# Kernel optimization log

Hardware: AMD Instinct MI355X
Metric: run time of the kernel (lower is better)

The kernel has to match this reference:

```python
import jax, jax.numpy as jnp
import numpy as np

B, N, D = 2, 4096, 512
H, DH = 8, 64  # heads, dim_head; inner_dim = H*DH = 512
SCALE = DH ** -0.5


def setup_inputs() -> dict:
    key = jax.random.key(0)
    ks = jax.random.split(key, 5)
    s = 0.02
    return {
        "x": jax.random.normal(ks[0], (B, N, D), dtype=jnp.float32),
        "Wq": jax.random.normal(ks[1], (D, H * DH), dtype=jnp.float32) * s,
        "Wk": jax.random.normal(ks[2], (D, H * DH), dtype=jnp.float32) * s,
        "Wv": jax.random.normal(ks[3], (D, H * DH), dtype=jnp.float32) * s,
        "Wo": jax.random.normal(ks[4], (H * DH, D), dtype=jnp.float32) * s,
        "bo": jnp.zeros((D,), dtype=jnp.float32),
    }


def reference(x, Wq, Wk, Wv, Wo, bo):
    b, n, _ = x.shape
    # projections (bias-free), then split heads: b n (h d) -> b h n d
    q = (x @ Wq).reshape(b, n, H, DH).transpose(0, 2, 1, 3)
    k = (x @ Wk).reshape(b, n, H, DH).transpose(0, 2, 1, 3)
    v = (x @ Wv).reshape(b, n, H, DH).transpose(0, 2, 1, 3)
    # fp32 QK^T (module upcasts under ATTN_PRECISION='fp32')
    sim = jnp.einsum("bhid,bhjd->bhij", q.astype(jnp.float32), k.astype(jnp.float32)) * SCALE
    attn = jax.nn.softmax(sim, axis=-1)
    out = jnp.einsum("bhij,bhjd->bhid", attn, v)
    # merge heads: b h n d -> b n (h d)
    out = out.transpose(0, 2, 1, 3).reshape(b, n, H * DH)
    return out @ Wo + bo  # dropout p=0 -> identity
```

## Files before the change

kernel.cpp:

```cpp
#include <hip/hip_runtime.h>


typedef __bf16 bf16;
typedef __bf16 bf16x2 __attribute__((ext_vector_type(2)));
typedef __bf16 bf16x4 __attribute__((ext_vector_type(4)));
typedef __bf16 bf16x8 __attribute__((ext_vector_type(8)));
typedef float  f32x2  __attribute__((ext_vector_type(2)));
typedef float  f32x4  __attribute__((ext_vector_type(4)));
typedef float  f32x16 __attribute__((ext_vector_type(16)));

#define MFMA16 __builtin_amdgcn_mfma_f32_16x16x32_bf16
#define MFMA32 __builtin_amdgcn_mfma_f32_32x32x16_bf16

__device__ __forceinline__ int swz(int b) { return b ^ ((b >> 3) & 0x70); }

__device__ __forceinline__ void gload16(const void* g, void* l) {
  __builtin_amdgcn_global_load_lds(
      (const __attribute__((address_space(1))) unsigned int*)g,
      (__attribute__((address_space(3))) unsigned int*)l, 16, 0, 0);
}

__device__ __forceinline__ unsigned pk2(float a, float b) {
  union { bf16x2 h; unsigned u; } x;
  x.h[0] = (bf16)a; x.h[1] = (bf16)b;
  return x.u;
}

__global__ __launch_bounds__(256) void k_cvt(const float* __restrict__ x,
                                             const float* __restrict__ Wq,
                                             const float* __restrict__ Wk,
                                             const float* __restrict__ Wv,
                                             const float* __restrict__ Wo,
                                             bf16* __restrict__ xb,
                                             bf16* __restrict__ Wts) {
  int bid = blockIdx.x;
  if (bid < 4096) {
    int i = (bid * 256 + threadIdx.x) * 4;
    f32x4 v = *(const f32x4*)(x + i);
    bf16x4 o;
    o[0] = (bf16)v[0]; o[1] = (bf16)v[1]; o[2] = (bf16)v[2]; o[3] = (bf16)v[3];
    *(bf16x4*)(xb + i) = o;
  } else {
    int t = (bid - 4096) * 256 + threadIdx.x;
    int w = t >> 18, idx = t & 262143;
    int k = idx >> 9, n = idx & 511;
    const float* W = (w == 0) ? Wq : (w == 1) ? Wk : (w == 2) ? Wv : Wo;
    Wts[(size_t)w * 262144 + n * 512 + k] = (bf16)W[k * 512 + n];
  }
}

__device__ __forceinline__ void gemm_mainloop(const char* Ag, const char* Bg,
                                              char* sA, char* sB, f32x4 acc[4][4]) {
  const int tid = threadIdx.x;
  const int g = (tid >> 4) & 3, lr = tid & 15;
  const int wr = ((tid >> 7) & 1) * 64, wc = ((tid >> 6) & 1) * 64;
  f32x4 zero = {0.f, 0.f, 0.f, 0.f};
#pragma unroll
  for (int mt = 0; mt < 4; mt++)
#pragma unroll
    for (int nt = 0; nt < 4; nt++) acc[mt][nt] = zero;

  for (int k0 = 0; k0 < 512; k0 += 64) {
#pragma unroll
    for (int i = 0; i < 4; i++) {
      int c = i * 256 + tid;
      int row = c >> 3, cl = (c & 7) ^ (row & 7);
      gload16(Ag + row * 1024 + k0 * 2 + cl * 16, sA + (c & ~63) * 16);
    }
#pragma unroll
    for (int i = 0; i < 4; i++) {
      int c = i * 256 + tid;
      int row = c >> 3, cl = (c & 7) ^ (row & 7);
      gload16(Bg + row * 1024 + k0 * 2 + cl * 16, sB + (c & ~63) * 16);
    }
    __syncthreads();
#pragma unroll
    for (int kk = 0; kk < 2; kk++) {
      bf16x8 af[4], bfr[4];
#pragma unroll
      for (int mt = 0; mt < 4; mt++)
        af[mt] = *(const bf16x8*)(sA + swz((wr + mt * 16 + lr) * 128 + kk * 64 + g * 16));
#pragma unroll
      for (int nt = 0; nt < 4; nt++)
        bfr[nt] = *(const bf16x8*)(sB + swz((wc + nt * 16 + lr) * 128 + kk * 64 + g * 16));
#pragma unroll
      for (int mt = 0; mt < 4; mt++)
#pragma unroll
        for (int nt = 0; nt < 4; nt++)
          acc[mt][nt] = MFMA16(af[mt], bfr[nt], acc[mt][nt], 0, 0, 0);
    }
    __syncthreads();
  }
}

__global__ __launch_bounds__(256) void k_gemm_qkv(const bf16* __restrict__ Xb,
                                                  const bf16* __restrict__ Wts,
                                                  bf16* __restrict__ Qo,
                                                  bf16* __restrict__ Ko,
                                                  bf16* __restrict__ Vto) {
  __shared__ __align__(16) char smem[32768];
  const int tid = threadIdx.x;
  const int g = (tid >> 4) & 3, lr = tid & 15;
  const int mb = blockIdx.x * 128, nb = blockIdx.y * 128;
  const int mode = blockIdx.z;
  f32x4 acc[4][4];
  gemm_mainloop((const char*)Xb + (size_t)mb * 1024,
                (const char*)(Wts + (size_t)mode * 262144) + (size_t)nb * 1024,
                smem, smem + 16384, acc);
  const int wr = ((tid >> 7) & 1) * 64, wc = ((tid >> 6) & 1) * 64;
  const float qs = 0.18033688011112042f;
#pragma unroll
  for (int mt = 0; mt < 4; mt++)
#pragma unroll
    for (int nt = 0; nt < 4; nt++)
#pragma unroll
      for (int r = 0; r < 4; r++) {
        int m = mb + wr + mt * 16 + g * 4 + r;
        int cc = nb + wc + nt * 16 + lr;
        float v = acc[mt][nt][r];
        int b = m >> 12, ns = m & 4095, h = cc >> 6, d = cc & 63;
        if (mode == 0)
          Qo[((size_t)(b * 8 + h) * 4096 + ns) * 64 + d] = (bf16)(v * qs);
        else if (mode == 1)
          Ko[((size_t)(b * 8 + h) * 4096 + ns) * 64 + d] = (bf16)v;
        else
          Vto[((size_t)(b * 8 + h) * 64 + d) * 4096 + ns] = (bf16)v;
      }
}

__global__ __launch_bounds__(256) void k_gemm_out(const bf16* __restrict__ Ob,
                                                  const bf16* __restrict__ WtO,
                                                  const float* __restrict__ bo,
                                                  float* __restrict__ out) {
  __shared__ __align__(16) char smem[32768];
  const int tid = threadIdx.x;
  const int g = (tid >> 4) & 3, lr = tid & 15;
  const int mb = blockIdx.x * 128, nb = blockIdx.y * 128;
  f32x4 acc[4][4];
  gemm_mainloop((const char*)Ob + (size_t)mb * 1024,
                (const char*)WtO + (size_t)nb * 1024, smem, smem + 16384, acc);
  const int wr = ((tid >> 7) & 1) * 64, wc = ((tid >> 6) & 1) * 64;
#pragma unroll
  for (int mt = 0; mt < 4; mt++)
#pragma unroll
    for (int nt = 0; nt < 4; nt++)
#pragma unroll
      for (int r = 0; r < 4; r++) {
        int m = mb + wr + mt * 16 + g * 4 + r;
        int cc = nb + wc + nt * 16 + lr;
        out[(size_t)m * 512 + cc] = acc[mt][nt][r] + bo[cc];
      }
}

__global__ __launch_bounds__(512, 4) void k_attn(const bf16* __restrict__ Q,
                                                 const bf16* __restrict__ K,
                                                 const bf16* __restrict__ Vt,
                                                 bf16* __restrict__ O) {
  __shared__ __align__(16) char smem[65536];
  const int tid = threadIdx.x;
  const int l = tid & 63, w = tid >> 6, lo = l & 31, hi = l >> 5;
  const int strip = w & 3, half = w >> 2;
  const int tid2 = tid & 255;
  const int bh = blockIdx.y;
  const int q0 = blockIdx.x * 128 + strip * 32;
  const char* Qp = (const char*)Q + ((size_t)bh * 4096 + q0 + lo) * 128;
  bf16x8 qf[4];
#pragma unroll
  for (int ks = 0; ks < 4; ks++) qf[ks] = *(const bf16x8*)(Qp + ks * 32 + hi * 16);

  const int srow = tid2 >> 3, scl = (tid2 & 7) ^ (srow & 7);
  const char* pK0 = (const char*)K + (size_t)bh * 4096 * 128 +
                    (size_t)half * 2048 * 128 + srow * 128 + scl * 16;
  const char* pV0 = (const char*)Vt + (size_t)bh * 64 * 8192 +
                    (size_t)half * 4096 + (size_t)srow * 8192 + scl * 16;
  char* lbase = smem + half * 32768;
  const int sdst = (tid2 & ~63) * 16;

  const int offR = swz(lo * 128 + hi * 16);

  f32x16 acc0 = {}, acc1 = {};
  const f32x16 z16 = {};
  float lsum = 0.f;

  {
    char* d = lbase + sdst;
    gload16(pK0, d);
    gload16(pK0 + 4096, d + 4096);
    gload16(pV0, d + 8192);
    gload16(pV0 + 262144, d + 12288);
  }
  pK0 += 8192; pV0 += 128;
  __syncthreads();

  for (int t = 0; t < 32; t++) {
    if (t < 31) {
      char* d = lbase + ((t + 1) & 1) * 16384 + sdst;
      gload16(pK0, d);
      gload16(pK0 + 4096, d + 4096);
      gload16(pV0, d + 8192);
      gload16(pV0 + 262144, d + 12288);
      pK0 += 8192; pV0 += 128;
    }
    const char* b0 = lbase + (t & 1) * 16384;
    const char* k0p = b0 + offR;
    const char* k1p = b0 + (offR ^ 32);
    const char* k2p = b0 + (offR ^ 64);
    const char* k3p = b0 + (offR ^ 96);
    f32x16 s0, s1;
    __builtin_amdgcn_s_setprio(1);
    s0 = MFMA32(*(const bf16x8*)(k0p), qf[0], z16, 0, 0, 0);
    s1 = MFMA32(*(const bf16x8*)(k0p + 4096), qf[0], z16, 0, 0, 0);
    s0 = MFMA32(*(const bf16x8*)(k1p), qf[1], s0, 0, 0, 0);
    s1 = MFMA32(*(const bf16x8*)(k1p + 4096), qf[1], s1, 0, 0, 0);
    s0 = MFMA32(*(const bf16x8*)(k2p), qf[2], s0, 0, 0, 0);
    s1 = MFMA32(*(const bf16x8*)(k2p + 4096), qf[2], s1, 0, 0, 0);
    s0 = MFMA32(*(const bf16x8*)(k3p), qf[3], s0, 0, 0, 0);
    s1 = MFMA32(*(const bf16x8*)(k3p + 4096), qf[3], s1, 0, 0, 0);
    __builtin_amdgcn_s_setprio(0);
#pragma unroll
    for (int r = 0; r < 16; r++) {
      s0[r] = __builtin_amdgcn_exp2f(s0[r]);
      s1[r] = __builtin_amdgcn_exp2f(s1[r]);
    }
    {
      float a0 = (s0[0] + s0[1]) + (s0[2] + s0[3]);
      float a1 = (s0[4] + s0[5]) + (s0[6] + s0[7]);
      float a2 = (s0[8] + s0[9]) + (s0[10] + s0[11]);
      float a3 = (s0[12] + s0[13]) + (s0[14] + s0[15]);
      float a4 = (s1[0] + s1[1]) + (s1[2] + s1[3]);
      float a5 = (s1[4] + s1[5]) + (s1[6] + s1[7]);
      float a6 = (s1[8] + s1[9]) + (s1[10] + s1[11]);
      float a7 = (s1[12] + s1[13]) + (s1[14] + s1[15]);
      float rs = ((a0 + a1) + (a2 + a3)) + ((a4 + a5) + (a6 + a7));
      rs += __shfl_xor(rs, 32, 64);
      lsum += rs;
    }
    union U8 { unsigned u[4]; bf16x8 v; };
    bf16x8 pa0, pa1, pa2, pa3;
    {
      unsigned A0 = pk2(s0[0], s0[1]), A1 = pk2(s0[2], s0[3]);
      unsigned B0 = pk2(s0[4], s0[5]), B1 = pk2(s0[6], s0[7]);
      asm("v_permlane32_swap_b32 %0, %1" : "+v"(A0), "+v"(B0));
      asm("v_permlane32_swap_b32 %0, %1" : "+v"(A1), "+v"(B1));
      U8 pu; pu.u[0] = A0; pu.u[1] = A1; pu.u[2] = B0; pu.u[3] = B1;
      pa0 = pu.v;
    }
    {
      unsigned A0 = pk2(s0[8], s0[9]), A1 = pk2(s0[10], s0[11]);
      unsigned B0 = pk2(s0[12], s0[13]), B1 = pk2(s0[14], s0[15]);
      asm("v_permlane32_swap_b32 %0, %1" : "+v"(A0), "+v"(B0));
      asm("v_permlane32_swap_b32 %0, %1" : "+v"(A1), "+v"(B1));
      U8 pu; pu.u[0] = A0; pu.u[1] = A1; pu.u[2] = B0; pu.u[3] = B1;
      pa1 = pu.v;
    }
    {
      unsigned A0 = pk2(s1[0], s1[1]), A1 = pk2(s1[2], s1[3]);
      unsigned B0 = pk2(s1[4], s1[5]), B1 = pk2(s1[6], s1[7]);
      asm("v_permlane32_swap_b32 %0, %1" : "+v"(A0), "+v"(B0));
      asm("v_permlane32_swap_b32 %0, %1" : "+v"(A1), "+v"(B1));
      U8 pu; pu.u[0] = A0; pu.u[1] = A1; pu.u[2] = B0; pu.u[3] = B1;
      pa2 = pu.v;
    }
    {
      unsigned A0 = pk2(s1[8], s1[9]), A1 = pk2(s1[10], s1[11]);
      unsigned B0 = pk2(s1[12], s1[13]), B1 = pk2(s1[14], s1[15]);
      asm("v_permlane32_swap_b32 %0, %1" : "+v"(A0), "+v"(B0));
      asm("v_permlane32_swap_b32 %0, %1" : "+v"(A1), "+v"(B1));
      U8 pu; pu.u[0] = A0; pu.u[1] = A1; pu.u[2] = B0; pu.u[3] = B1;
      pa3 = pu.v;
    }
    __builtin_amdgcn_s_setprio(1);
    acc0 = MFMA32(pa0, *(const bf16x8*)(k0p + 8192), acc0, 0, 0, 0);
    acc1 = MFMA32(pa0, *(const bf16x8*)(k0p + 12288), acc1, 0, 0, 0);
    acc0 = MFMA32(pa1, *(const bf16x8*)(k1p + 8192), acc0, 0, 0, 0);
    acc1 = MFMA32(pa1, *(const bf16x8*)(k1p + 12288), acc1, 0, 0, 0);
    acc0 = MFMA32(pa2, *(const bf16x8*)(k2p + 8192), acc0, 0, 0, 0);
    acc1 = MFMA32(pa2, *(const bf16x8*)(k2p + 12288), acc1, 0, 0, 0);
    acc0 = MFMA32(pa3, *(const bf16x8*)(k3p + 8192), acc0, 0, 0, 0);
    acc1 = MFMA32(pa3, *(const bf16x8*)(k3p + 12288), acc1, 0, 0, 0);
    __builtin_amdgcn_s_setprio(0);
    __syncthreads();
  }
  float* accStash = (float*)smem;
  float* lArr = (float*)(smem + 32768);
  float* cArr = (float*)(smem + 36864);
  if (l < 32) lArr[w * 32 + lo] = lsum;
  __syncthreads();
  if (l < 32) {
    float lP = lArr[(w ^ 4) * 32 + lo];
    cArr[w * 32 + lo] = 1.0f / (lsum + lP);
  }
  __syncthreads();
  if (half == 1) {
#pragma unroll
    for (int r = 0; r < 16; r++) {
      int qrow = (r & 3) + 8 * (r >> 2) + 4 * hi;
      float cf = cArr[w * 32 + qrow];
      accStash[(strip * 32 + qrow) * 64 + lo] = acc0[r] * cf;
      accStash[(strip * 32 + qrow) * 64 + lo + 32] = acc1[r] * cf;
    }
  }
  __syncthreads();
  if (half == 0) {
    const int b = bh >> 3, h = bh & 7;
#pragma unroll
    for (int r = 0; r < 16; r++) {
      int qrow = (r & 3) + 8 * (r >> 2) + 4 * hi;
      float cf = cArr[w * 32 + qrow];
      float o0 = acc0[r] * cf + accStash[(strip * 32 + qrow) * 64 + lo];
      float o1 = acc1[r] * cf + accStash[(strip * 32 + qrow) * 64 + lo + 32];
      size_t base = ((size_t)b * 4096 + q0 + qrow) * 512 + h * 64 + lo;
      O[base] = (bf16)o0;
      O[base + 32] = (bf16)o1;
    }
  }
}

extern "C" void kernel_launch(void* const* d_in, const int* in_sizes, int n_in,
                              void* d_out, int out_size, void* d_ws, size_t ws_size,
                              hipStream_t stream) {
  (void)in_sizes; (void)n_in; (void)out_size; (void)ws_size;
  const float* x  = (const float*)d_in[0];
  const float* Wq = (const float*)d_in[1];
  const float* Wk = (const float*)d_in[2];
  const float* Wv = (const float*)d_in[3];
  const float* Wo = (const float*)d_in[4];
  const float* bo = (const float*)d_in[5];
  float* out = (float*)d_out;
  char* ws = (char*)d_ws;
  bf16* Xb  = (bf16*)(ws);
  bf16* Wts = (bf16*)(ws + 8388608);
  bf16* Qb  = (bf16*)(ws + 10485760);
  bf16* Kb  = (bf16*)(ws + 18874368);
  bf16* Vtb = (bf16*)(ws + 27262976);
  bf16* Ob  = (bf16*)(ws + 35651584);

  hipLaunchKernelGGL(k_cvt, dim3(8192), dim3(256), 0, stream,
                     x, Wq, Wk, Wv, Wo, Xb, Wts);
  hipLaunchKernelGGL(k_gemm_qkv, dim3(64, 4, 3), dim3(256), 0, stream,
                     Xb, Wts, Qb, Kb, Vtb);
  hipLaunchKernelGGL(k_attn, dim3(32, 16), dim3(512), 0, stream, Qb, Kb, Vtb, Ob);
  hipLaunchKernelGGL(k_gemm_out, dim3(64, 4), dim3(256), 0, stream,
                     Ob, Wts + 3 * 262144, bo, out);
}
```

Baseline: 137.6 us.

## Shrink output GEMM tiles and overlap attention K/V prefetch with waitcnt barriers

The output projection GEMM now uses 64x128 tiles with its own inline mainloop, launching twice as many blocks (512 instead of 256) to fill more CUs. The attention loop swaps the end-of-iteration __syncthreads for explicit s_barrier plus s_waitcnt vmcnt(4). This lets the next tile's K/V loads stay in flight while the current tile is consumed. The risk is that the output GEMM mainloop is not double-buffered, and the manual vmcnt counting must stay correct.

```diff
diff --git a/kernel.cpp b/kernel.cpp
--- a/kernel.cpp
+++ b/kernel.cpp
@@ -132,16 +132,55 @@
                                                   const bf16* __restrict__ WtO,
                                                   const float* __restrict__ bo,
                                                   float* __restrict__ out) {
-  __shared__ __align__(16) char smem[32768];
+  __shared__ __align__(16) char smem[24576];
+  char* sA = smem;
+  char* sB = smem + 8192;
   const int tid = threadIdx.x;
   const int g = (tid >> 4) & 3, lr = tid & 15;
-  const int mb = blockIdx.x * 128, nb = blockIdx.y * 128;
-  f32x4 acc[4][4];
-  gemm_mainloop((const char*)Ob + (size_t)mb * 1024,
-                (const char*)WtO + (size_t)nb * 1024, smem, smem + 16384, acc);
-  const int wr = ((tid >> 7) & 1) * 64, wc = ((tid >> 6) & 1) * 64;
-#pragma unroll
-  for (int mt = 0; mt < 4; mt++)
+  const int wr = ((tid >> 7) & 1) * 32, wc = ((tid >> 6) & 1) * 64;
+  const int mb = blockIdx.x * 64, nb = blockIdx.y * 128;
+  const char* Ag = (const char*)Ob + (size_t)mb * 1024;
+  const char* Bg = (const char*)WtO + (size_t)nb * 1024;
+  f32x4 acc[2][4];
+  f32x4 zero = {0.f, 0.f, 0.f, 0.f};
+#pragma unroll
+  for (int mt = 0; mt < 2; mt++)
+#pragma unroll
+    for (int nt = 0; nt < 4; nt++) acc[mt][nt] = zero;
+
+  for (int k0 = 0; k0 < 512; k0 += 64) {
+#pragma unroll
+    for (int i = 0; i < 2; i++) {
+      int c = i * 256 + tid;
+      int row = c >> 3, cl = (c & 7) ^ (row & 7);
+      gload16(Ag + row * 1024 + k0 * 2 + cl * 16, sA + (c & ~63) * 16);
+    }
+#pragma unroll
+    for (int i = 0; i < 4; i++) {
+      int c = i * 256 + tid;
+      int row = c >> 3, cl = (c & 7) ^ (row & 7);
+      gload16(Bg + row * 1024 + k0 * 2 + cl * 16, sB + (c & ~63) * 16);
+    }
+    __syncthreads();
+#pragma unroll
+    for (int kk = 0; kk < 2; kk++) {
+      bf16x8 af[2], bfr[4];
+#pragma unroll
+      for (int mt = 0; mt < 2; mt++)
+        af[mt] = *(const bf16x8*)(sA + swz((wr + mt * 16 + lr) * 128 + kk * 64 + g * 16));
+#pragma unroll
+      for (int nt = 0; nt < 4; nt++)
+        bfr[nt] = *(const bf16x8*)(sB + swz((wc + nt * 16 + lr) * 128 + kk * 64 + g * 16));
+#pragma unroll
+      for (int mt = 0; mt < 2; mt++)
+#pragma unroll
+        for (int nt = 0; nt < 4; nt++)
+          acc[mt][nt] = MFMA16(af[mt], bfr[nt], acc[mt][nt], 0, 0, 0);
+    }
+    __syncthreads();
+  }
+#pragma unroll
+  for (int mt = 0; mt < 2; mt++)
 #pragma unroll
     for (int nt = 0; nt < 4; nt++)
 #pragma unroll
@@ -190,9 +229,9 @@
     gload16(pV0 + 262144, d + 12288);
   }
   pK0 += 8192; pV0 += 128;
-  __syncthreads();
 
   for (int t = 0; t < 32; t++) {
+    __builtin_amdgcn_s_barrier();
     if (t < 31) {
       char* d = lbase + ((t + 1) & 1) * 16384 + sdst;
       gload16(pK0, d);
@@ -200,7 +239,12 @@
       gload16(pV0, d + 8192);
       gload16(pV0 + 262144, d + 12288);
       pK0 += 8192; pV0 += 128;
-    }
+      asm volatile("s_waitcnt vmcnt(4)" ::: "memory");
+    } else {
+      asm volatile("s_waitcnt vmcnt(0)" ::: "memory");
+    }
+    __builtin_amdgcn_s_barrier();
+    __builtin_amdgcn_sched_barrier(0);
     const char* b0 = lbase + (t & 1) * 16384;
     const char* k0p = b0 + offR;
     const char* k1p = b0 + (offR ^ 32);
@@ -279,8 +323,8 @@
     acc0 = MFMA32(pa3, *(const bf16x8*)(k3p + 8192), acc0, 0, 0, 0);
     acc1 = MFMA32(pa3, *(const bf16x8*)(k3p + 12288), acc1, 0, 0, 0);
     __builtin_amdgcn_s_setprio(0);
-    __syncthreads();
-  }
+  }
+  __syncthreads();
   float* accStash = (float*)smem;
   float* lArr = (float*)(smem + 32768);
   float* cArr = (float*)(smem + 36864);
@@ -340,6 +384,6 @@
   hipLaunchKernelGGL(k_gemm_qkv, dim3(64, 4, 3), dim3(256), 0, stream,
                      Xb, Wts, Qb, Kb, Vtb);
   hipLaunchKernelGGL(k_attn, dim3(32, 16), dim3(512), 0, stream, Qb, Kb, Vtb, Ob);
-  hipLaunchKernelGGL(k_gemm_out, dim3(64, 4), dim3(256), 0, stream,
+  hipLaunchKernelGGL(k_gemm_out, dim3(128, 4), dim3(256), 0, stream,
                      Ob, Wts + 3 * 262144, bo, out);
 }
```

New measurement: 136.4 us. About the same (-0.9%).
